# Performance work log

Measured on AMD Instinct MI355X. Metric: run time of the kernel, lower is better.

Reference implementation:

```python
import jax, jax.numpy as jnp
from jax import lax
import numpy as np

B, L_IN, C_IN, C_MARK = 4, 1024, 7, 4
D, H, DK, DFF, NL = 512, 8, 64, 2048, 4
WINDOW = [4, 4, 4]
INNER = 5


def _get_mask(input_size, window_size, inner_size):
    all_size = [input_size]
    for w in window_size:
        all_size.append(all_size[-1] // w)
    L = sum(all_size)
    m = np.zeros((L, L), dtype=np.float32)
    iw = inner_size // 2
    for li in range(len(all_size)):
        start = sum(all_size[:li])
        for i in range(start, start + all_size[li]):
            m[i, max(i - iw, start):min(i + iw + 1, start + all_size[li])] = 1
    for li in range(1, len(all_size)):
        start = sum(all_size[:li])
        for i in range(start, start + all_size[li]):
            ls = start - all_size[li - 1] + (i - start) * window_size[li - 1]
            if i == start + all_size[li] - 1:
                rs = start
            else:
                rs = start - all_size[li - 1] + (i - start + 1) * window_size[li - 1]
            m[i, ls:rs] = 1
            m[ls:rs, i] = 1
    return (1 - m).astype(bool), all_size


def _refer_points(all_sizes, window_size):
    n = all_sizes[0]
    idx = np.zeros((n, len(all_sizes)), dtype=np.int64)
    for i in range(n):
        idx[i, 0] = i
        former = i
        for j in range(1, len(all_sizes)):
            start = sum(all_sizes[:j])
            inner = former - (start - all_sizes[j - 1])
            former = start + min(inner // window_size[j - 1], all_sizes[j] - 1)
            idx[i, j] = former
    return idx


def _pos_emb(L, d):
    pos = np.arange(L, dtype=np.float32)[:, None]
    div = np.exp(np.arange(0, d, 2, dtype=np.float32) * (-np.log(10000.0) / d))
    pe = np.zeros((L, d), dtype=np.float32)
    pe[:, 0::2] = np.sin(pos * div)
    pe[:, 1::2] = np.cos(pos * div)
    return pe


def _ln(x, g, b, eps=1e-5):
    mu = x.mean(-1, keepdims=True)
    v = ((x - mu) ** 2).mean(-1, keepdims=True)
    return (x - mu) * lax.rsqrt(v + eps) * g + b


def setup_inputs() -> dict:
    key = jax.random.key(0)
    ks = iter(jax.random.split(key, 64))

    def nrm(shape, fan_in):
        return jax.random.normal(next(ks), shape, jnp.float32) / np.float32(np.sqrt(fan_in))

    return dict(
        x_enc=jax.random.normal(next(ks), (B, L_IN, C_IN), jnp.float32),
        x_mark=jax.random.uniform(next(ks), (B, L_IN, C_MARK), jnp.float32),
        conv_w=nrm((D, C_IN, 3), C_IN * 3), conv_b=jnp.zeros((D,), jnp.float32),
        temp_w=nrm((C_MARK, D), C_MARK), temp_b=jnp.zeros((D,), jnp.float32),
        down_w=nrm((D, DK), D), down_b=jnp.zeros((DK,), jnp.float32),
        pyr_conv_w=nrm((3, DK, DK, WINDOW[0]), DK * WINDOW[0]),
        pyr_conv_b=jnp.zeros((3, DK), jnp.float32),
        bn_g=jnp.ones((3, DK), jnp.float32), bn_b=jnp.zeros((3, DK), jnp.float32),
        up_w=nrm((DK, D), DK), up_b=jnp.zeros((D,), jnp.float32),
        norm_g=jnp.ones((D,), jnp.float32), norm_b=jnp.zeros((D,), jnp.float32),
        wq=nrm((NL, D, H * DK), D), wk=nrm((NL, D, H * DK), D), wv=nrm((NL, D, H * DK), D),
        fc_w=nrm((NL, H * DK, D), H * DK), fc_b=jnp.zeros((NL, D), jnp.float32),
        ln1_g=jnp.ones((NL, D), jnp.float32), ln1_b=jnp.zeros((NL, D), jnp.float32),
        w1=nrm((NL, D, DFF), D), b1=jnp.zeros((NL, DFF), jnp.float32),
        w2=nrm((NL, DFF, D), DFF), b2=jnp.zeros((NL, D), jnp.float32),
        ln2_g=jnp.ones((NL, D), jnp.float32), ln2_b=jnp.zeros((NL, D), jnp.float32),
    )


def reference(x_enc, x_mark, conv_w, conv_b, temp_w, temp_b, down_w, down_b,
              pyr_conv_w, pyr_conv_b, bn_g, bn_b, up_w, up_b, norm_g, norm_b,
              wq, wk, wv, fc_w, fc_b, ln1_g, ln1_b, w1, b1, w2, b2, ln2_g, ln2_b):
    mask_np, all_size = _get_mask(L_IN, WINDOW, INNER)
    mask = jnp.asarray(mask_np)                      # (L_tot, L_tot) bool, True = blocked
    idx = jnp.asarray(_refer_points(all_size, WINDOW))  # (L_IN, n_levels)
    pe = jnp.asarray(_pos_emb(L_IN, D))
    L_tot = sum(all_size)

    # --- DataEmbedding: circular Conv1d token emb + positional + temporal linear ---
    xt = jnp.transpose(x_enc, (0, 2, 1))             # (B, C_IN, L)
    xt = jnp.concatenate([xt[:, :, -1:], xt, xt[:, :, :1]], axis=-1)  # circular pad=1
    val = lax.conv_general_dilated(xt, conv_w, (1,), 'VALID',
                                   dimension_numbers=('NCH', 'OIH', 'NCH'))
    val = jnp.transpose(val, (0, 2, 1)) + conv_b
    seq = val + pe[None] + x_mark @ temp_w + temp_b  # (B, L_IN, D); dropout = eval no-op

    # --- Bottleneck_Construct: build pyramid levels with strided convs ---
    tmp = jnp.transpose(seq @ down_w + down_b, (0, 2, 1))  # (B, DK, L_IN)
    outs = []
    for i in range(len(WINDOW)):
        tmp = lax.conv_general_dilated(tmp, pyr_conv_w[i], (WINDOW[i],), 'VALID',
                                       dimension_numbers=('NCH', 'OIH', 'NCH'))
        tmp = tmp + pyr_conv_b[i][None, :, None]
        # BatchNorm1d at eval with running stats (0,1): affine only
        tmp = jax.nn.elu(tmp * bn_g[i][None, :, None] + bn_b[i][None, :, None])
        outs.append(tmp)
    pyr = jnp.transpose(jnp.concatenate(outs, axis=2), (0, 2, 1)) @ up_w + up_b
    seq = _ln(jnp.concatenate([seq, pyr], axis=1), norm_g, norm_b)  # (B, L_tot, D)

    temperature = float(np.sqrt(DK))
    for l in range(NL):
        # post-norm multi-head attention with pyramidal boolean mask
        res = seq
        q = (seq @ wq[l]).reshape(B, L_tot, H, DK)
        k = (seq @ wk[l]).reshape(B, L_tot, H, DK)
        v = (seq @ wv[l]).reshape(B, L_tot, H, DK)
        att = jnp.einsum('bqhd,bkhd->bhqk', q / temperature, k)
        att = jnp.where(mask[None, None], jnp.float32(-1e9), att)
        p = jax.nn.softmax(att, axis=-1)
        o = jnp.einsum('bhqk,bkhd->bqhd', p, v).reshape(B, L_tot, H * DK)
        seq = _ln(o @ fc_w[l] + fc_b[l] + res, ln1_g[l], ln1_b[l])
        # post-norm FFN (exact gelu, as F.gelu)
        res = seq
        hmid = jax.nn.gelu(seq @ w1[l] + b1[l], approximate=False)
        seq = _ln(hmid @ w2[l] + b2[l] + res, ln2_g[l], ln2_b[l])

    # --- refer_points gather: concat all pyramid levels per input position ---
    out = seq[:, idx, :]                             # (B, L_IN, n_levels, D)
    return out.reshape(B, L_IN, -1)                  # (B, L_IN, n_levels*D)
```

## Files before the change

kernel.cpp:

```cpp
#include <hip/hip_runtime.h>
#include <hip/hip_bf16.h>
#include <math.h>


typedef __attribute__((ext_vector_type(8))) short short8;
typedef __attribute__((ext_vector_type(4))) float f32x4;

__device__ inline ushort f2bf(float x) {
  union { __hip_bfloat16 h; ushort u; } cv; cv.h = __float2bfloat16(x); return cv.u;
}
__device__ inline float bf2f(ushort u) {
  union { unsigned int i; float f; } cv; cv.i = (unsigned)u << 16; return cv.f;
}
__device__ inline float lo16(unsigned u) { union { unsigned i; float f; } c; c.i = u << 16; return c.f; }
__device__ inline float hi16(unsigned u) { union { unsigned i; float f; } c; c.i = u & 0xffff0000u; return c.f; }
__device__ inline unsigned pack2(float a, float b) {
  return (unsigned)f2bf(a) | ((unsigned)f2bf(b) << 16);
}

__device__ inline float gelu_f(float x) {
  float y = 0.7978845608028654f * (x + 0.044715f * x * x * x);
  float t = __expf(-2.0f * y);
  float th = (1.0f - t) / (1.0f + t);
  return 0.5f * x * (1.0f + th);
}

__device__ inline int xcd_chunk(int orig, int nwg) {
  int q = nwg >> 3, r = nwg & 7;
  int xcd = orig & 7, idx = orig >> 3;
  int base = (xcd < r) ? xcd * (q + 1) : r * (q + 1) + (xcd - r) * q;
  return base + idx;
}

#define GLD16(gp, lp)                                                        \
  __builtin_amdgcn_global_load_lds(                                          \
      (const __attribute__((address_space(1))) void*)(gp),                   \
      (__attribute__((address_space(3))) void*)(lp), 16, 0, 0)

__global__ __launch_bounds__(512) void embed_kernel(
    const float* __restrict__ x_enc, const float* __restrict__ x_mark,
    const float* __restrict__ conv_w, const float* __restrict__ conv_b,
    const float* __restrict__ temp_w, const float* __restrict__ temp_b,
    float* __restrict__ e, ushort* __restrict__ e_bf) {
  int bl = blockIdx.x;
  int b = bl >> 10, l = bl & 1023;
  int d = threadIdx.x;
  int lm1 = (l + 1023) & 1023;
  int lp1 = (l + 1) & 1023;
  const float* w  = conv_w + d * 21;
  const float* x0 = x_enc + (size_t)(b * 1024 + lm1) * 7;
  const float* x1 = x_enc + (size_t)(b * 1024 + l)   * 7;
  const float* x2 = x_enc + (size_t)(b * 1024 + lp1) * 7;
  float acc = conv_b[d];
#pragma unroll
  for (int ci = 0; ci < 7; ci++) {
    acc = fmaf(x0[ci], w[ci * 3 + 0], acc);
    acc = fmaf(x1[ci], w[ci * 3 + 1], acc);
    acc = fmaf(x2[ci], w[ci * 3 + 2], acc);
  }
  int j = d >> 1;
  float dv = expf((float)(2 * j) * (-9.210340371976184f / 512.0f));
  float ang = (float)l * dv;
  float pe = (d & 1) ? cosf(ang) : sinf(ang);
  const float* xm = x_mark + (size_t)(b * 1024 + l) * 4;
  float mk = temp_b[d];
  mk = fmaf(xm[0], temp_w[d],        mk);
  mk = fmaf(xm[1], temp_w[512 + d],  mk);
  mk = fmaf(xm[2], temp_w[1024 + d], mk);
  mk = fmaf(xm[3], temp_w[1536 + d], mk);
  float v = acc + pe + mk;
  e[(size_t)bl * 512 + d] = v;
  e_bf[(size_t)bl * 512 + d] = f2bf(v);
}

__global__ __launch_bounds__(256) void transpose_cast(
    const float* __restrict__ src, ushort* __restrict__ dst,
    int K, int N, size_t src_lstride, size_t dst_lstride) {
  src += (size_t)blockIdx.z * src_lstride;
  dst += (size_t)blockIdx.z * dst_lstride;
  __shared__ float t[32][33];
  int k0 = blockIdx.y * 32, n0 = blockIdx.x * 32;
  int tx = threadIdx.x, ty = threadIdx.y;
#pragma unroll
  for (int i = 0; i < 4; i++)
    t[ty + i * 8][tx] = src[(size_t)(k0 + ty + i * 8) * N + n0 + tx];
  __syncthreads();
#pragma unroll
  for (int i = 0; i < 4; i++)
    dst[(size_t)(n0 + ty + i * 8) * K + k0 + tx] = f2bf(t[tx][ty + i * 8]);
}

__global__ __launch_bounds__(256) void gemm_bf16_t64(
    const ushort* __restrict__ A, const ushort* __restrict__ Bt,
    const float* __restrict__ bias, ushort* __restrict__ C,
    int N, int K, int act) {
  __shared__ short As[2][4096];
  __shared__ short Bs[2][4096];
  int nbx = N >> 6;
  int wgid = xcd_chunk(blockIdx.x, gridDim.x);
  int bx = wgid % nbx, by = wgid / nbx;
  int tid = threadIdx.x;
  int w = tid >> 6, lane = tid & 63;
  int bm = by << 6, bn = bx << 6;
  int gch = (tid & 7) ^ ((tid >> 3) & 7);
  const short* Ab = (const short*)A + (size_t)(bm + (tid >> 3)) * K + gch * 8;
  const short* Bb = (const short*)Bt + (size_t)(bn + (tid >> 3)) * K + gch * 8;
  int ldst = (tid & 192) * 8;
  int wr = (w >> 1) << 5, wc = (w & 1) << 5;
  int lr = lane & 15, kg = lane >> 4;
  int cs0 = ((kg)     ^ (lane & 7)) * 8;
  int cs1 = ((4 + kg) ^ (lane & 7)) * 8;
  f32x4 acc[2][2] = {};
#define STG64(buf, kt) do {                                                  \
    GLD16(Ab + (kt),                  &As[buf][ldst]);                       \
    GLD16(Ab + (kt) + (size_t)32 * K, &As[buf][2048 + ldst]);                \
    GLD16(Bb + (kt),                  &Bs[buf][ldst]);                       \
    GLD16(Bb + (kt) + (size_t)32 * K, &Bs[buf][2048 + ldst]); } while (0)
  STG64(0, 0);
  __syncthreads();
  int nt = K >> 6;
  for (int t = 0; t < nt; t++) {
    int cur = t & 1;
    if (t + 1 < nt) STG64(cur ^ 1, (t + 1) << 6);
    short8 a_[2][2], b_[2][2];
#pragma unroll
    for (int m = 0; m < 2; m++) {
      int rb = (wr + m * 16 + lr) * 64;
      a_[m][0] = *(const short8*)&As[cur][rb + cs0];
      a_[m][1] = *(const short8*)&As[cur][rb + cs1];
    }
#pragma unroll
    for (int n = 0; n < 2; n++) {
      int rb = (wc + n * 16 + lr) * 64;
      b_[n][0] = *(const short8*)&Bs[cur][rb + cs0];
      b_[n][1] = *(const short8*)&Bs[cur][rb + cs1];
    }
#pragma unroll
    for (int ks = 0; ks < 2; ks++)
#pragma unroll
      for (int m = 0; m < 2; m++)
#pragma unroll
        for (int n = 0; n < 2; n++)
          acc[m][n] = __builtin_amdgcn_mfma_f32_16x16x32_bf16(a_[m][ks], b_[n][ks], acc[m][n], 0, 0, 0);
    __syncthreads();
  }
#undef STG64
  int r0 = bm + wr + kg * 4;
  int c0 = bn + wc + lr;
#pragma unroll
  for (int m = 0; m < 2; m++) {
#pragma unroll
    for (int n = 0; n < 2; n++) {
      int col = c0 + n * 16;
      float bv = bias ? bias[col] : 0.0f;
#pragma unroll
      for (int j = 0; j < 4; j++) {
        int row = r0 + m * 16 + j;
        float v = acc[m][n][j] + bv;
        if (act == 1) v = gelu_f(v);
        C[(size_t)row * N + col] = f2bf(v);
      }
    }
  }
}

__global__ __launch_bounds__(256) void gemm_bf16_t32(
    const ushort* __restrict__ A, const ushort* __restrict__ Bt,
    const float* __restrict__ bias, ushort* __restrict__ C,
    int N, int K) {
  __shared__ short As[2][2048];
  __shared__ short Bs[2][4096];
  int nbx = N >> 6;
  int wgid = xcd_chunk(blockIdx.x, gridDim.x);
  int bx = wgid % nbx, by = wgid / nbx;
  int tid = threadIdx.x;
  int w = tid >> 6, lane = tid & 63;
  int bm = by << 5, bn = bx << 6;
  int gch = (tid & 7) ^ ((tid >> 3) & 7);
  const short* Ab = (const short*)A + (size_t)(bm + (tid >> 3)) * K + gch * 8;
  const short* Bb = (const short*)Bt + (size_t)(bn + (tid >> 3)) * K + gch * 8;
  int ldst = (tid & 192) * 8;
  int wr = (w >> 1) << 4, wc = (w & 1) << 5;
  int lr = lane & 15, kg = lane >> 4;
  int cs0 = ((kg)     ^ (lane & 7)) * 8;
  int cs1 = ((4 + kg) ^ (lane & 7)) * 8;
  f32x4 acc[2] = {};
#define STG32(buf, kt) do {                                                  \
    GLD16(Ab + (kt),                  &As[buf][ldst]);                       \
    GLD16(Bb + (kt),                  &Bs[buf][ldst]);                       \
    GLD16(Bb + (kt) + (size_t)32 * K, &Bs[buf][2048 + ldst]); } while (0)
  STG32(0, 0);
  __syncthreads();
  int nt = K >> 6;
  for (int t = 0; t < nt; t++) {
    int cur = t & 1;
    if (t + 1 < nt) STG32(cur ^ 1, (t + 1) << 6);
    short8 a_[2], b_[2][2];
    {
      int rb = (wr + lr) * 64;
      a_[0] = *(const short8*)&As[cur][rb + cs0];
      a_[1] = *(const short8*)&As[cur][rb + cs1];
    }
#pragma unroll
    for (int n = 0; n < 2; n++) {
      int rb = (wc + n * 16 + lr) * 64;
      b_[n][0] = *(const short8*)&Bs[cur][rb + cs0];
      b_[n][1] = *(const short8*)&Bs[cur][rb + cs1];
    }
#pragma unroll
    for (int ks = 0; ks < 2; ks++)
#pragma unroll
      for (int n = 0; n < 2; n++)
        acc[n] = __builtin_amdgcn_mfma_f32_16x16x32_bf16(a_[ks], b_[n][ks], acc[n], 0, 0, 0);
    __syncthreads();
  }
#undef STG32
  int r0 = bm + wr + kg * 4;
  int c0 = bn + wc + lr;
#pragma unroll
  for (int n = 0; n < 2; n++) {
    int col = c0 + n * 16;
    float bv = bias ? bias[col] : 0.0f;
#pragma unroll
    for (int j = 0; j < 4; j++) {
      int row = r0 + j;
      C[(size_t)row * N + col] = f2bf(acc[n][j] + bv);
    }
  }
}

__global__ __launch_bounds__(64) void pyr_conv(
    const ushort* __restrict__ in, int in_base, int in_bstr,
    ushort* __restrict__ out, int out_base, int out_bstr, int out_len,
    const float* __restrict__ w, const float* __restrict__ bias,
    const float* __restrict__ bng, const float* __restrict__ bnb) {
  int blk = blockIdx.x;
  int b = blk / out_len, to = blk - b * out_len;
  int co = threadIdx.x;
  __shared__ float xin[4][64];
  const ushort* src = in + (size_t)(b * in_bstr + in_base + 4 * to) * 64;
#pragma unroll
  for (int r2 = 0; r2 < 4; r2++) xin[r2][co] = bf2f(src[r2 * 64 + co]);
  __syncthreads();
  const float* wr = w + (size_t)co * 256;
  float acc = bias[co];
#pragma unroll 16
  for (int ci = 0; ci < 64; ci++) {
    acc = fmaf(xin[0][ci], wr[ci * 4 + 0], acc);
    acc = fmaf(xin[1][ci], wr[ci * 4 + 1], acc);
    acc = fmaf(xin[2][ci], wr[ci * 4 + 2], acc);
    acc = fmaf(xin[3][ci], wr[ci * 4 + 3], acc);
  }
  float y = fmaf(bng[co], acc, bnb[co]);
  y = y > 0.0f ? y : expm1f(y);
  out[(size_t)(b * out_bstr + out_base + to) * 64 + co] = f2bf(y);
}

__global__ __launch_bounds__(256) void ln_concat(
    const float* __restrict__ e, const ushort* __restrict__ pyru,
    const float* __restrict__ g, const float* __restrict__ bta,
    ushort* __restrict__ seq_bf) {
  int r = (blockIdx.x << 2) + (threadIdx.x >> 6);
  int lane = threadIdx.x & 63;
  int b = r / 1360, i = r - b * 1360;
  int c = lane << 3;
  float v[8];
  if (i < 1024) {
    const float* src = e + (size_t)(b * 1024 + i) * 512 + c;
    float4 v0 = *(const float4*)&src[0];
    float4 v1 = *(const float4*)&src[4];
    v[0] = v0.x; v[1] = v0.y; v[2] = v0.z; v[3] = v0.w;
    v[4] = v1.x; v[5] = v1.y; v[6] = v1.z; v[7] = v1.w;
  } else {
    uint4 sv = *(const uint4*)(pyru + (size_t)(b * 336 + (i - 1024)) * 512 + c);
    v[0] = lo16(sv.x); v[1] = hi16(sv.x); v[2] = lo16(sv.y); v[3] = hi16(sv.y);
    v[4] = lo16(sv.z); v[5] = hi16(sv.z); v[6] = lo16(sv.w); v[7] = hi16(sv.w);
  }
  float sum = v[0]+v[1]+v[2]+v[3]+v[4]+v[5]+v[6]+v[7];
#pragma unroll
  for (int off = 1; off < 64; off <<= 1) sum += __shfl_xor(sum, off);
  float mu = sum * (1.0f / 512.0f);
  float sq = 0.0f;
#pragma unroll
  for (int k = 0; k < 8; k++) { v[k] -= mu; sq += v[k] * v[k]; }
#pragma unroll
  for (int off = 1; off < 64; off <<= 1) sq += __shfl_xor(sq, off);
  float inv = rsqrtf(sq * (1.0f / 512.0f) + 1e-5f);
  float4 g0 = *(const float4*)&g[c],   g1 = *(const float4*)&g[c + 4];
  float4 b0 = *(const float4*)&bta[c], b1 = *(const float4*)&bta[c + 4];
  uint4 pk;
  pk.x = pack2(v[0]*inv*g0.x + b0.x, v[1]*inv*g0.y + b0.y);
  pk.y = pack2(v[2]*inv*g0.z + b0.z, v[3]*inv*g0.w + b0.w);
  pk.z = pack2(v[4]*inv*g1.x + b1.x, v[5]*inv*g1.y + b1.y);
  pk.w = pack2(v[6]*inv*g1.z + b1.z, v[7]*inv*g1.w + b1.w);
  *(uint4*)(seq_bf + (size_t)r * 512 + c) = pk;
}

__global__ __launch_bounds__(256) void ln_add(
    ushort* __restrict__ seq_bf, const ushort* __restrict__ t1,
    const float* __restrict__ g, const float* __restrict__ bta) {
  int r = (blockIdx.x << 2) + (threadIdx.x >> 6);
  int lane = threadIdx.x & 63;
  int c = lane << 3;
  ushort* row = seq_bf + (size_t)r * 512 + c;
  uint4 sv = *(const uint4*)row;
  uint4 tv = *(const uint4*)(t1 + (size_t)r * 512 + c);
  float v[8] = {
    lo16(sv.x) + lo16(tv.x), hi16(sv.x) + hi16(tv.x),
    lo16(sv.y) + lo16(tv.y), hi16(sv.y) + hi16(tv.y),
    lo16(sv.z) + lo16(tv.z), hi16(sv.z) + hi16(tv.z),
    lo16(sv.w) + lo16(tv.w), hi16(sv.w) + hi16(tv.w) };
  float sum = v[0]+v[1]+v[2]+v[3]+v[4]+v[5]+v[6]+v[7];
#pragma unroll
  for (int off = 1; off < 64; off <<= 1) sum += __shfl_xor(sum, off);
  float mu = sum * (1.0f / 512.0f);
  float sq = 0.0f;
#pragma unroll
  for (int k = 0; k < 8; k++) { v[k] -= mu; sq += v[k] * v[k]; }
#pragma unroll
  for (int off = 1; off < 64; off <<= 1) sq += __shfl_xor(sq, off);
  float inv = rsqrtf(sq * (1.0f / 512.0f) + 1e-5f);
  float4 g0 = *(const float4*)&g[c],   g1 = *(const float4*)&g[c + 4];
  float4 b0 = *(const float4*)&bta[c], b1 = *(const float4*)&bta[c + 4];
  uint4 pk;
  pk.x = pack2(v[0]*inv*g0.x + b0.x, v[1]*inv*g0.y + b0.y);
  pk.y = pack2(v[2]*inv*g0.z + b0.z, v[3]*inv*g0.w + b0.w);
  pk.z = pack2(v[4]*inv*g1.x + b1.x, v[5]*inv*g1.y + b1.y);
  pk.w = pack2(v[6]*inv*g1.z + b1.z, v[7]*inv*g1.w + b1.w);
  *(uint4*)row = pk;
}

__global__ __launch_bounds__(512) void attn_sparse(
    const ushort* __restrict__ qkv, ushort* __restrict__ o) {
  int r = blockIdx.x;
  int b = r / 1360, i = r - b * 1360;
  int h = threadIdx.x >> 6, lane = threadIdx.x & 63;
  int S, sz, li;
  if (i < 1024)      { li = 0; S = 0;    sz = 1024; }
  else if (i < 1280) { li = 1; S = 1024; sz = 256; }
  else if (i < 1344) { li = 2; S = 1280; sz = 64; }
  else               { li = 3; S = 1344; sz = 16; }
  int p = i - S;
  int lo = p - 2; if (lo < 0) lo = 0;
  int hi = p + 2; if (hi > sz - 1) hi = sz - 1;
  int cnt = hi - lo + 1;
  int nk = cnt + (li > 0 ? 4 : 0) + (li < 3 ? 1 : 0);
  int Sprev = (li == 1) ? 0 : (li == 2) ? 1024 : 1280;
  int Snext = (li == 0) ? 1024 : (li == 1) ? 1280 : 1344;
  int j2 = lane >> 2, c = lane & 3;
  int key;
  if (j2 < cnt)                      key = S + lo + j2;
  else if (li > 0 && j2 - cnt < 4)   key = Sprev + 4 * p + (j2 - cnt);
  else if (li < 3)                   key = Snext + (p >> 2);
  else                               key = S + p;
  float partial = 0.0f;
  {
    const uint4* qv = (const uint4*)(qkv + (size_t)r * 1536 + h * 64 + c * 16);
    const uint4* kv = (const uint4*)(qkv + (size_t)(b * 1360 + key) * 1536 + 512 + h * 64 + c * 16);
#pragma unroll
    for (int cc = 0; cc < 2; cc++) {
      uint4 a = qv[cc], k4 = kv[cc];
      partial = fmaf(lo16(a.x), lo16(k4.x), partial); partial = fmaf(hi16(a.x), hi16(k4.x), partial);
      partial = fmaf(lo16(a.y), lo16(k4.y), partial); partial = fmaf(hi16(a.y), hi16(k4.y), partial);
      partial = fmaf(lo16(a.z), lo16(k4.z), partial); partial = fmaf(hi16(a.z), hi16(k4.z), partial);
      partial = fmaf(lo16(a.w), lo16(k4.w), partial); partial = fmaf(hi16(a.w), hi16(k4.w), partial);
    }
  }
  partial += __shfl_xor(partial, 1);
  partial += __shfl_xor(partial, 2);
  float s = partial * 0.125f;
  float m = -1e30f;
  for (int j = 0; j < nk; j++) m = fmaxf(m, __shfl(s, 4 * j));
  float denom = 0.0f;
  for (int j = 0; j < nk; j++) denom += __expf(__shfl(s, 4 * j) - m);
  float inv = 1.0f / denom;
  float acc = 0.0f;
  for (int j = 0; j < nk; j++) {
    float pj = __expf(__shfl(s, 4 * j) - m) * inv;
    int kj = __shfl(key, 4 * j);
    float vv = bf2f(qkv[(size_t)(b * 1360 + kj) * 1536 + 1024 + h * 64 + lane]);
    acc = fmaf(pj, vv, acc);
  }
  o[(size_t)r * 512 + h * 64 + lane] = f2bf(acc);
}

__global__ __launch_bounds__(512) void gather_out(
    const ushort* __restrict__ seq_bf, float* __restrict__ out) {
  int bl = blockIdx.x;
  int b = bl >> 10, i = bl & 1023;
  int d = threadIdx.x;
  size_t ob = (size_t)bl * 2048 + d;
  size_t base = (size_t)b * 1360;
  out[ob]        = bf2f(seq_bf[(base + i) * 512 + d]);
  out[ob + 512]  = bf2f(seq_bf[(base + 1024 + (i >> 2)) * 512 + d]);
  out[ob + 1024] = bf2f(seq_bf[(base + 1280 + (i >> 4)) * 512 + d]);
  out[ob + 1536] = bf2f(seq_bf[(base + 1344 + (i >> 6)) * 512 + d]);
}

extern "C" void kernel_launch(void* const* d_in, const int* in_sizes, int n_in,
                              void* d_out, int out_size, void* d_ws, size_t ws_size,
                              hipStream_t stream) {
  const float* x_enc   = (const float*)d_in[0];
  const float* x_mark  = (const float*)d_in[1];
  const float* conv_w  = (const float*)d_in[2];
  const float* conv_b  = (const float*)d_in[3];
  const float* temp_w  = (const float*)d_in[4];
  const float* temp_b  = (const float*)d_in[5];
  const float* down_w  = (const float*)d_in[6];
  const float* down_b  = (const float*)d_in[7];
  const float* pyr_w   = (const float*)d_in[8];
  const float* pyr_b   = (const float*)d_in[9];
  const float* bn_g    = (const float*)d_in[10];
  const float* bn_b    = (const float*)d_in[11];
  const float* up_w    = (const float*)d_in[12];
  const float* up_b    = (const float*)d_in[13];
  const float* norm_g  = (const float*)d_in[14];
  const float* norm_b  = (const float*)d_in[15];
  const float* wq      = (const float*)d_in[16];
  const float* wk      = (const float*)d_in[17];
  const float* wv      = (const float*)d_in[18];
  const float* fc_w    = (const float*)d_in[19];
  const float* fc_b    = (const float*)d_in[20];
  const float* ln1_g   = (const float*)d_in[21];
  const float* ln1_b   = (const float*)d_in[22];
  const float* w1      = (const float*)d_in[23];
  const float* b1      = (const float*)d_in[24];
  const float* w2      = (const float*)d_in[25];
  const float* b2      = (const float*)d_in[26];
  const float* ln2_g   = (const float*)d_in[27];
  const float* ln2_b   = (const float*)d_in[28];

  float* ws = (float*)d_ws;
  float*  e       = ws;
  ushort* e_bf    = (ushort*)(ws + 2097152);
  ushort* tmp0_bf = (ushort*)(ws + 3145728);
  ushort* pyrf_bf = (ushort*)(ws + 3276800);
  ushort* pyru_bf = (ushort*)(ws + 3319808);
  ushort* qkv_bf = (ushort*)ws;
  ushort* o_bf   = (ushort*)(ws + 4227072);
  ushort* th_bf  = (ushort*)ws;
  ushort* t1     = (ushort*)(ws + 5636096);
  ushort* dwt    = (ushort*)(ws + 7045120);
  ushort* uwt    = (ushort*)(ws + 7061504);
  ushort* seq_bf = (ushort*)(ws + 11272192);
  ushort* qkvw   = (ushort*)(ws + 12681216);
  ushort* fcw    = (ushort*)(ws + 14254080);
  ushort* w1t    = (ushort*)(ws + 14778368);
  ushort* w2t    = (ushort*)(ws + 16875520);

  dim3 tb(32, 8);
  transpose_cast<<<dim3(16, 16, 4), tb, 0, stream>>>(wq, qkvw,          512, 512,  262144, 786432);
  transpose_cast<<<dim3(16, 16, 4), tb, 0, stream>>>(wk, qkvw + 262144, 512, 512,  262144, 786432);
  transpose_cast<<<dim3(16, 16, 4), tb, 0, stream>>>(wv, qkvw + 524288, 512, 512,  262144, 786432);
  transpose_cast<<<dim3(16, 16, 4), tb, 0, stream>>>(fc_w, fcw,         512, 512,  262144, 262144);
  transpose_cast<<<dim3(64, 16, 4), tb, 0, stream>>>(w1, w1t,           512, 2048, 1048576, 1048576);
  transpose_cast<<<dim3(16, 64, 4), tb, 0, stream>>>(w2, w2t,           2048, 512, 1048576, 1048576);
  transpose_cast<<<dim3(2, 16, 1), tb, 0, stream>>>(down_w, dwt,        512, 64,   0, 0);
  transpose_cast<<<dim3(16, 2, 1), tb, 0, stream>>>(up_w, uwt,          64, 512,   0, 0);

  embed_kernel<<<4096, 512, 0, stream>>>(x_enc, x_mark, conv_w, conv_b,
                                         temp_w, temp_b, e, e_bf);
  gemm_bf16_t32<<<128, 256, 0, stream>>>(e_bf, dwt, down_b, tmp0_bf, 64, 512);
  pyr_conv<<<4 * 256, 64, 0, stream>>>(tmp0_bf, 0, 1024, pyrf_bf, 0, 336, 256,
                                       pyr_w, pyr_b, bn_g, bn_b);
  pyr_conv<<<4 * 64, 64, 0, stream>>>(pyrf_bf, 0, 336, pyrf_bf, 256, 336, 64,
                                      pyr_w + 16384, pyr_b + 64, bn_g + 64, bn_b + 64);
  pyr_conv<<<4 * 16, 64, 0, stream>>>(pyrf_bf, 256, 336, pyrf_bf, 320, 336, 16,
                                      pyr_w + 32768, pyr_b + 128, bn_g + 128, bn_b + 128);
  gemm_bf16_t32<<<8 * 42, 256, 0, stream>>>(pyrf_bf, uwt, up_b, pyru_bf, 512, 64);
  ln_concat<<<1360, 256, 0, stream>>>(e, pyru_bf, norm_g, norm_b, seq_bf);

  for (int l = 0; l < 4; l++) {
    gemm_bf16_t64<<<24 * 86, 256, 0, stream>>>(seq_bf, qkvw + (size_t)l * 786432,
                                               nullptr, qkv_bf, 1536, 512, 0);
    attn_sparse<<<5440, 512, 0, stream>>>(qkv_bf, o_bf);
    gemm_bf16_t32<<<8 * 172, 256, 0, stream>>>(o_bf, fcw + (size_t)l * 262144,
                                               fc_b + l * 512, t1, 512, 512);
    ln_add<<<1360, 256, 0, stream>>>(seq_bf, t1, ln1_g + l * 512, ln1_b + l * 512);
    gemm_bf16_t64<<<32 * 86, 256, 0, stream>>>(seq_bf, w1t + (size_t)l * 1048576,
                                               b1 + l * 2048, th_bf, 2048, 512, 1);
    gemm_bf16_t32<<<8 * 172, 256, 0, stream>>>(th_bf, w2t + (size_t)l * 1048576,
                                               b2 + l * 512, t1, 512, 2048);
    ln_add<<<1360, 256, 0, stream>>>(seq_bf, t1, ln2_g + l * 512, ln2_b + l * 512);
  }
  gather_out<<<4096, 512, 0, stream>>>(seq_bf, (float*)d_out);
}
```

Measured before the change: 541.8 us.

## Use 8-wave GEMM tiles, shuffle-tree softmax, vectorized gather, fast trig in embed

The 64x64 GEMM now runs 512 threads (8 waves), each wave owning a 16x32 sub-tile, so every thread issues half as many global-to-LDS copies and keeps fewer accumulators. The aim is more waves per CU to hide latency. The sparse attention softmax replaces serial loops over keys with xor-shuffle max and sum reductions, and it computes each exp once per key instead of twice. The output gather switches to 8-byte loads and float4 stores, and the positional embedding uses the fast intrinsic exp, sin and cos at some cost in accuracy.

```diff
diff --git a/kernel.cpp b/kernel.cpp
--- a/kernel.cpp
+++ b/kernel.cpp
@@ -59,9 +59,9 @@
     acc = fmaf(x2[ci], w[ci * 3 + 2], acc);
   }
   int j = d >> 1;
-  float dv = expf((float)(2 * j) * (-9.210340371976184f / 512.0f));
+  float dv = __expf((float)(2 * j) * (-9.210340371976184f / 512.0f));
   float ang = (float)l * dv;
-  float pe = (d & 1) ? cosf(ang) : sinf(ang);
+  float pe = (d & 1) ? __cosf(ang) : __sinf(ang);
   const float* xm = x_mark + (size_t)(b * 1024 + l) * 4;
   float mk = temp_b[d];
   mk = fmaf(xm[0], temp_w[d],        mk);
@@ -90,7 +90,7 @@
     dst[(size_t)(n0 + ty + i * 8) * K + k0 + tx] = f2bf(t[tx][ty + i * 8]);
 }
 
-__global__ __launch_bounds__(256) void gemm_bf16_t64(
+__global__ __launch_bounds__(512, 8) void gemm_bf16_t64w8(
     const ushort* __restrict__ A, const ushort* __restrict__ Bt,
     const float* __restrict__ bias, ushort* __restrict__ C,
     int N, int K, int act) {
@@ -105,29 +105,26 @@
   int gch = (tid & 7) ^ ((tid >> 3) & 7);
   const short* Ab = (const short*)A + (size_t)(bm + (tid >> 3)) * K + gch * 8;
   const short* Bb = (const short*)Bt + (size_t)(bn + (tid >> 3)) * K + gch * 8;
-  int ldst = (tid & 192) * 8;
-  int wr = (w >> 1) << 5, wc = (w & 1) << 5;
+  int ldst = (tid & 448) * 8;
+  int wr = (w & 3) << 4, wc = (w >> 2) << 5;
   int lr = lane & 15, kg = lane >> 4;
   int cs0 = ((kg)     ^ (lane & 7)) * 8;
   int cs1 = ((4 + kg) ^ (lane & 7)) * 8;
-  f32x4 acc[2][2] = {};
-#define STG64(buf, kt) do {                                                  \
-    GLD16(Ab + (kt),                  &As[buf][ldst]);                       \
-    GLD16(Ab + (kt) + (size_t)32 * K, &As[buf][2048 + ldst]);                \
-    GLD16(Bb + (kt),                  &Bs[buf][ldst]);                       \
-    GLD16(Bb + (kt) + (size_t)32 * K, &Bs[buf][2048 + ldst]); } while (0)
-  STG64(0, 0);
+  f32x4 acc[2] = {};
+#define STG(buf, kt) do {                                                    \
+    GLD16(Ab + (kt), &As[buf][ldst]);                                        \
+    GLD16(Bb + (kt), &Bs[buf][ldst]); } while (0)
+  STG(0, 0);
   __syncthreads();
   int nt = K >> 6;
   for (int t = 0; t < nt; t++) {
     int cur = t & 1;
-    if (t + 1 < nt) STG64(cur ^ 1, (t + 1) << 6);
-    short8 a_[2][2], b_[2][2];
-#pragma unroll
-    for (int m = 0; m < 2; m++) {
-      int rb = (wr + m * 16 + lr) * 64;
-      a_[m][0] = *(const short8*)&As[cur][rb + cs0];
-      a_[m][1] = *(const short8*)&As[cur][rb + cs1];
+    if (t + 1 < nt) STG(cur ^ 1, (t + 1) << 6);
+    short8 a_[2], b_[2][2];
+    {
+      int rb = (wr + lr) * 64;
+      a_[0] = *(const short8*)&As[cur][rb + cs0];
+      a_[1] = *(const short8*)&As[cur][rb + cs1];
     }
 #pragma unroll
     for (int n = 0; n < 2; n++) {
@@ -138,28 +135,23 @@
 #pragma unroll
     for (int ks = 0; ks < 2; ks++)
 #pragma unroll
-      for (int m = 0; m < 2; m++)
-#pragma unroll
-        for (int n = 0; n < 2; n++)
-          acc[m][n] = __builtin_amdgcn_mfma_f32_16x16x32_bf16(a_[m][ks], b_[n][ks], acc[m][n], 0, 0, 0);
+      for (int n = 0; n < 2; n++)
+        acc[n] = __builtin_amdgcn_mfma_f32_16x16x32_bf16(a_[ks], b_[n][ks], acc[n], 0, 0, 0);
     __syncthreads();
   }
-#undef STG64
+#undef STG
   int r0 = bm + wr + kg * 4;
   int c0 = bn + wc + lr;
 #pragma unroll
-  for (int m = 0; m < 2; m++) {
-#pragma unroll
-    for (int n = 0; n < 2; n++) {
-      int col = c0 + n * 16;
-      float bv = bias ? bias[col] : 0.0f;
-#pragma unroll
-      for (int j = 0; j < 4; j++) {
-        int row = r0 + m * 16 + j;
-        float v = acc[m][n][j] + bv;
-        if (act == 1) v = gelu_f(v);
-        C[(size_t)row * N + col] = f2bf(v);
-      }
+  for (int n = 0; n < 2; n++) {
+    int col = c0 + n * 16;
+    float bv = bias ? bias[col] : 0.0f;
+#pragma unroll
+    for (int j = 0; j < 4; j++) {
+      int row = r0 + j;
+      float v = acc[n][j] + bv;
+      if (act == 1) v = gelu_f(v);
+      C[(size_t)row * N + col] = f2bf(v);
     }
   }
 }
@@ -368,15 +360,22 @@
   }
   partial += __shfl_xor(partial, 1);
   partial += __shfl_xor(partial, 2);
-  float s = partial * 0.125f;
-  float m = -1e30f;
-  for (int j = 0; j < nk; j++) m = fmaxf(m, __shfl(s, 4 * j));
-  float denom = 0.0f;
-  for (int j = 0; j < nk; j++) denom += __expf(__shfl(s, 4 * j) - m);
-  float inv = 1.0f / denom;
+  float s = (j2 < nk) ? partial * 0.125f : -1e30f;
+  float m = s;
+  m = fmaxf(m, __shfl_xor(m, 4));
+  m = fmaxf(m, __shfl_xor(m, 8));
+  m = fmaxf(m, __shfl_xor(m, 16));
+  m = fmaxf(m, __shfl_xor(m, 32));
+  float ev = __expf(s - m);
+  float den = ev;
+  den += __shfl_xor(den, 4);
+  den += __shfl_xor(den, 8);
+  den += __shfl_xor(den, 16);
+  den += __shfl_xor(den, 32);
+  float inv = 1.0f / den;
   float acc = 0.0f;
   for (int j = 0; j < nk; j++) {
-    float pj = __expf(__shfl(s, 4 * j) - m) * inv;
+    float pj = __shfl(ev, 4 * j) * inv;
     int kj = __shfl(key, 4 * j);
     float vv = bf2f(qkv[(size_t)(b * 1360 + kj) * 1536 + 1024 + h * 64 + lane]);
     acc = fmaf(pj, vv, acc);
@@ -388,13 +387,19 @@
     const ushort* __restrict__ seq_bf, float* __restrict__ out) {
   int bl = blockIdx.x;
   int b = bl >> 10, i = bl & 1023;
-  int d = threadIdx.x;
-  size_t ob = (size_t)bl * 2048 + d;
+  int t = threadIdx.x;
+  int q = t >> 7, e4 = (t & 127) << 2;
+  int src_row = (q == 0) ? i
+              : (q == 1) ? 1024 + (i >> 2)
+              : (q == 2) ? 1280 + (i >> 4)
+              :            1344 + (i >> 6);
   size_t base = (size_t)b * 1360;
-  out[ob]        = bf2f(seq_bf[(base + i) * 512 + d]);
-  out[ob + 512]  = bf2f(seq_bf[(base + 1024 + (i >> 2)) * 512 + d]);
-  out[ob + 1024] = bf2f(seq_bf[(base + 1280 + (i >> 4)) * 512 + d]);
-  out[ob + 1536] = bf2f(seq_bf[(base + 1344 + (i >> 6)) * 512 + d]);
+  const ushort* sp = seq_bf + ((base + src_row) * 512 + e4);
+  uint2 sv = *(const uint2*)sp;
+  float4 ov;
+  ov.x = lo16(sv.x); ov.y = hi16(sv.x);
+  ov.z = lo16(sv.y); ov.w = hi16(sv.y);
+  *(float4*)&out[(size_t)bl * 2048 + q * 512 + e4] = ov;
 }
 
 extern "C" void kernel_launch(void* const* d_in, const int* in_sizes, int n_in,
@@ -471,14 +476,14 @@
   ln_concat<<<1360, 256, 0, stream>>>(e, pyru_bf, norm_g, norm_b, seq_bf);
 
   for (int l = 0; l < 4; l++) {
-    gemm_bf16_t64<<<24 * 86, 256, 0, stream>>>(seq_bf, qkvw + (size_t)l * 786432,
-                                               nullptr, qkv_bf, 1536, 512, 0);
+    gemm_bf16_t64w8<<<24 * 86, 512, 0, stream>>>(seq_bf, qkvw + (size_t)l * 786432,
+                                                 nullptr, qkv_bf, 1536, 512, 0);
     attn_sparse<<<5440, 512, 0, stream>>>(qkv_bf, o_bf);
     gemm_bf16_t32<<<8 * 172, 256, 0, stream>>>(o_bf, fcw + (size_t)l * 262144,
                                                fc_b + l * 512, t1, 512, 512);
     ln_add<<<1360, 256, 0, stream>>>(seq_bf, t1, ln1_g + l * 512, ln1_b + l * 512);
-    gemm_bf16_t64<<<32 * 86, 256, 0, stream>>>(seq_bf, w1t + (size_t)l * 1048576,
-                                               b1 + l * 2048, th_bf, 2048, 512, 1);
+    gemm_bf16_t64w8<<<32 * 86, 512, 0, stream>>>(seq_bf, w1t + (size_t)l * 1048576,
+                                                 b1 + l * 2048, th_bf, 2048, 512, 1);
     gemm_bf16_t32<<<8 * 172, 256, 0, stream>>>(th_bf, w2t + (size_t)l * 1048576,
                                                b2 + l * 512, t1, 512, 2048);
     ln_add<<<1360, 256, 0, stream>>>(seq_bf, t1, ln2_g + l * 512, ln2_b + l * 512);
```

Measured after the change: 521.3 us. -3.8%, faster.
